# Optimization experiments

Measured on AMD Instinct MI355X. Metric: run time of the kernel, lower is better.

Reference implementation:

```python
import jax, jax.numpy as jnp
import numpy as np

D_MODEL = 1024
NUM_HEADS = 16
D_KEY = D_MODEL // NUM_HEADS


def setup_inputs() -> dict:
    key = jax.random.key(0)
    ks = jax.random.split(key, 9)
    B, S = 2, 2048
    s = 1.0 / np.sqrt(D_MODEL)
    return {
        "x": jax.random.normal(ks[0], (B, S, D_MODEL), dtype=jnp.float32),
        "W_q": jax.random.normal(ks[1], (D_MODEL, D_MODEL), dtype=jnp.float32) * s,
        "b_q": jnp.zeros((D_MODEL,), dtype=jnp.float32),
        "W_k": jax.random.normal(ks[2], (D_MODEL, D_MODEL), dtype=jnp.float32) * s,
        "b_k": jnp.zeros((D_MODEL,), dtype=jnp.float32),
        "W_v": jax.random.normal(ks[3], (D_MODEL, D_MODEL), dtype=jnp.float32) * s,
        "b_v": jnp.zeros((D_MODEL,), dtype=jnp.float32),
        "W_o": jax.random.normal(ks[4], (D_MODEL, D_MODEL), dtype=jnp.float32) * s,
        "b_o": jnp.zeros((D_MODEL,), dtype=jnp.float32),
    }


def reference(x, W_q, b_q, W_k, b_k, W_v, b_v, W_o, b_o):
    B, S, _ = x.shape
    # Linear projections (torch nn.Linear: x @ W.T + b; here W stored as [in, out])
    Q = x @ W_q + b_q
    K = x @ W_k + b_k
    V = x @ W_v + b_v
    # [B, S, H, dk] -> [B, H, S, dk]
    def split_heads(t):
        return t.reshape(B, S, NUM_HEADS, D_KEY).transpose(0, 2, 1, 3)
    Q, K, V = split_heads(Q), split_heads(K), split_heads(V)
    scale = 1.0 / np.sqrt(D_KEY).astype(np.float32)
    logits = jnp.einsum("bhqd,bhkd->bhqk", Q, K) * scale  # [B,H,S,S]
    weights = jax.nn.softmax(logits, axis=-1)
    ctx = jnp.einsum("bhqk,bhkd->bhqd", weights, V)       # [B,H,S,dk]
    concat = ctx.transpose(0, 2, 1, 3).reshape(B, S, D_MODEL)
    return concat @ W_o + b_o
```

## Files before the change

kernel.cpp:

```cpp
#include <hip/hip_runtime.h>
#include <cstdint>
#include <cstddef>

#define SEQ   2048
#define NH    16
#define DK    64
#define DM    1024
#define MTOT  4096
#define QSCALE (0.125f * 1.44269504088896f)

typedef __attribute__((ext_vector_type(8))) short           short8;
typedef __attribute__((ext_vector_type(8))) unsigned short  ushort8;
typedef __attribute__((ext_vector_type(4))) unsigned short  ushort4v;
typedef __attribute__((ext_vector_type(2))) unsigned int    uint2v;
typedef __attribute__((ext_vector_type(4))) unsigned int    uint4v;
typedef __attribute__((ext_vector_type(4))) float           float4v;
typedef unsigned short u16;
typedef unsigned int   u32;

__device__ inline float4v mfma16(short8 a, short8 b, float4v c) {
    return __builtin_amdgcn_mfma_f32_16x16x32_bf16(a, b, c, 0, 0, 0);
}
__device__ inline u16 f2bf(float f) {
    u32 u = __float_as_uint(f);
    u += 0x7fffu + ((u >> 16) & 1u);
    return (u16)(u >> 16);
}
__device__ inline u32 pkbf(float a, float b) {
    u32 r;
    asm("v_cvt_pk_bf16_f32 %0, %1, %2" : "=v"(r) : "v"(a), "v"(b));
    return r;
}
__device__ inline float ex2(float x) {
    float r;
    asm("v_exp_f32 %0, %1" : "=v"(r) : "v"(x));
    return r;
}
__device__ inline void pl32swap(u32& a, u32& b) {
    asm("v_permlane32_swap_b32 %0, %1" : "+v"(a), "+v"(b));
}
__device__ inline void pl16swap(u32& a, u32& b) {
    asm("v_permlane16_swap_b32 %0, %1" : "+v"(a), "+v"(b));
}
__device__ inline void gld16(const void* g, void* lds) {
    __builtin_amdgcn_global_load_lds(
        (const __attribute__((address_space(1))) u32*)g,
        (__attribute__((address_space(3))) u32*)lds, 16, 0, 0);
}

__global__ __launch_bounds__(256)
void convert_x(const float* __restrict__ x, u16* __restrict__ xb)
{
    const int i = blockIdx.x * 256 + threadIdx.x;
    const float4v a = ((const float4v*)x)[2 * i];
    const float4v b = ((const float4v*)x)[2 * i + 1];
    ushort8 o;
    #pragma unroll
    for (int j = 0; j < 4; j++) { o[j] = f2bf(a[j]); o[4 + j] = f2bf(b[j]); }
    ((ushort8*)xb)[i] = o;
}

__global__ __launch_bounds__(256)
void transpose_w(const float* __restrict__ W0, const float* __restrict__ W1,
                 const float* __restrict__ W2, const float* __restrict__ W3,
                 u16* __restrict__ T0, u16* __restrict__ T1,
                 u16* __restrict__ T2, u16* __restrict__ T3)
{
    __shared__ u16 t[64][68];
    const float* W; u16* T;
    switch (blockIdx.z) {
        case 0: W = W0; T = T0; break;
        case 1: W = W1; T = T1; break;
        case 2: W = W2; T = T2; break;
        default: W = W3; T = T3; break;
    }
    const int n0 = blockIdx.x * 64, k0 = blockIdx.y * 64;
    const int r  = threadIdx.x >> 4;
    const int c4 = (threadIdx.x & 15) * 4;
    #pragma unroll
    for (int i = 0; i < 4; i++) {
        float4v v = *(const float4v*)&W[(size_t)(k0 + r + i * 16) * DM + n0 + c4];
        #pragma unroll
        for (int j = 0; j < 4; j++) t[r + i * 16][c4 + j] = f2bf(v[j]);
    }
    __syncthreads();
    #pragma unroll
    for (int i = 0; i < 4; i++) {
        const int rr = r + i * 16;
        ushort4v o;
        #pragma unroll
        for (int j = 0; j < 4; j++) o[j] = t[c4 + j][rr];
        *(ushort4v*)&T[(size_t)(n0 + rr) * DM + k0 + c4] = o;
    }
}

template<int TM, int MODE>
__global__ __launch_bounds__(512)
void gemm_bt(const u16* __restrict__ A, const u16* __restrict__ WT,
             const float* __restrict__ bq, const float* __restrict__ bk,
             const float* __restrict__ bv,
             void* __restrict__ out0, u16* __restrict__ outK, u16* __restrict__ outV)
{
    constexpr int NT = 512;
    constexpr int MF = TM / 32;
    __shared__ u16 Al[2][TM][64];
    __shared__ u16 Bl[2][128][64];
    const int tid  = threadIdx.x;
    const int lane = tid & 63, w = tid >> 6;
    const int quad = lane >> 4, l16 = lane & 15;

    const int nxb  = gridDim.x;
    const int wgid = blockIdx.y * nxb + blockIdx.x;
    const int per  = (nxb * gridDim.y) >> 3;
    const int nl   = (wgid & 7) * per + (wgid >> 3);
    const int n0 = (nl % nxb) * 128, m0 = (nl / nxb) * TM;

    const int wm = (w >> 2) * (TM / 2);
    const int wn = (w & 3) * 32;

    float4v acc[MF][2] = {};

    auto STAGE = [&](int k0, int buf) {
        #pragma unroll
        for (int j = 0; j < TM * 8 / NT; j++) {
            const int c = j * NT + tid;
            const int row = c >> 3, kc = c & 7;
            gld16(A + (size_t)(m0 + row) * DM + k0 + ((kc ^ (row & 7)) * 8),
                  &Al[buf][0][0] + (size_t)(j * NT + w * 64) * 8);
        }
        #pragma unroll
        for (int j = 0; j < 1024 / NT; j++) {
            const int c = j * NT + tid;
            const int row = c >> 3, kc = c & 7;
            gld16(WT + (size_t)(n0 + row) * DM + k0 + ((kc ^ (row & 7)) * 8),
                  &Bl[buf][0][0] + (size_t)(j * NT + w * 64) * 8);
        }
    };

    STAGE(0, 0);
    for (int ks = 0; ks < DM / 64; ++ks) {
        const int buf = ks & 1;
        __syncthreads();
        if (ks + 1 < DM / 64) STAGE((ks + 1) * 64, buf ^ 1);
        #pragma unroll
        for (int u = 0; u < 2; u++) {
            short8 af[MF], bf[2];
            #pragma unroll
            for (int mi = 0; mi < MF; mi++) {
                const int row = wm + mi * 16 + l16;
                af[mi] = *(const short8*)&Al[buf][row][((4 * u + quad) ^ (row & 7)) * 8];
            }
            #pragma unroll
            for (int ni = 0; ni < 2; ni++) {
                const int row = wn + ni * 16 + l16;
                bf[ni] = *(const short8*)&Bl[buf][row][((4 * u + quad) ^ (row & 7)) * 8];
            }
            __builtin_amdgcn_s_setprio(1);
            #pragma unroll
            for (int mi = 0; mi < MF; mi++)
                #pragma unroll
                for (int ni = 0; ni < 2; ni++)
                    acc[mi][ni] = mfma16(af[mi], bf[ni], acc[mi][ni]);
            __builtin_amdgcn_s_setprio(0);
        }
    }

    if constexpr (MODE == 0) {
        float* out = (float*)out0;
        #pragma unroll
        for (int ni = 0; ni < 2; ni++) {
            const int col = n0 + wn + ni * 16 + l16;
            const float bb = bq[col];
            #pragma unroll
            for (int mi = 0; mi < MF; mi++)
                #pragma unroll
                for (int r = 0; r < 4; r++) {
                    const int row = m0 + wm + mi * 16 + quad * 4 + r;
                    out[(size_t)row * DM + col] = acc[mi][ni][r] + bb;
                }
        }
    } else {
        const int seg = n0 >> 10;
        u16* outp = (seg == 0) ? (u16*)out0 : (seg == 1 ? outK : outV);
        const float* bias = (seg == 0) ? bq : (seg == 1 ? bk : bv);
        const float scl = (seg == 0) ? QSCALE : 1.0f;
        if (seg < 2) {
            #pragma unroll
            for (int ni = 0; ni < 2; ni++) {
                const int col = (n0 & 1023) + wn + ni * 16 + l16;
                const float bb = bias[col];
                const int h = col >> 6, d = col & 63;
                #pragma unroll
                for (int mi = 0; mi < MF; mi++)
                    #pragma unroll
                    for (int r = 0; r < 4; r++) {
                        const int row = m0 + wm + mi * 16 + quad * 4 + r;
                        const int b = row >> 11, s = row & (SEQ - 1);
                        outp[(((size_t)(b * NH + h) * SEQ + s) << 6) + d] =
                            f2bf((acc[mi][ni][r] + bb) * scl);
                    }
            }
        } else {
            #pragma unroll
            for (int ni = 0; ni < 2; ni++) {
                const int col = (n0 & 1023) + wn + ni * 16 + l16;
                const float bb = bias[col];
                const int h = col >> 6, d = col & 63;
                #pragma unroll
                for (int mi = 0; mi < MF; mi++) {
                    const int row0 = m0 + wm + mi * 16 + quad * 4;
                    const int b = row0 >> 11, s = row0 & (SEQ - 1);
                    uint2v pv;
                    pv[0] = pkbf(acc[mi][ni][0] + bb, acc[mi][ni][1] + bb);
                    pv[1] = pkbf(acc[mi][ni][2] + bb, acc[mi][ni][3] + bb);
                    *(uint2v*)&outp[(((size_t)((b * NH + h) * DK + d)) << 11) + s] = pv;
                }
            }
        }
    }
}

__global__ __launch_bounds__(512, 4)
void attn_kernel(const u16* __restrict__ Q, const u16* __restrict__ K,
                 const u16* __restrict__ VT, u16* __restrict__ Ctx)
{
    __shared__ __align__(16) u16 pool[32768];

    const int tid  = threadIdx.x;
    const int lane = tid & 63, w = tid >> 6;
    const int wq = w & 3, wgrp = w >> 2;
    const int quad = lane >> 4, l16 = lane & 15;

    const int wgid = blockIdx.y * 16 + blockIdx.x;
    const int nlin = (wgid & 7) * 64 + (wgid >> 3);
    const int qt = nlin & 15;
    const int bh = nlin >> 4;
    const size_t head = (size_t)bh * SEQ * DK;

    short8 qf[2][2];
    #pragma unroll
    for (int g = 0; g < 2; g++) {
        const size_t qrow = head + (size_t)(qt * 128 + wq * 32 + g * 16 + l16) * DK;
        qf[g][0] = *(const short8*)(Q + qrow + quad * 8);
        qf[g][1] = *(const short8*)(Q + qrow + 32 + quad * 8);
    }

    float4v acc[2][4] = {};
    float l_part[2] = {0.f, 0.f};

    const int sh = tid >> 8;
    const int rK = (tid >> 3) & 31, cK = tid & 7;
    const int dV = (tid >> 2) & 63, cV = tid & 3;
    const int sVk = (dV & 3) ^ ((dV >> 2) & 3);
    const u16* const Kg = K  + head + (size_t)(sh * 1024 + rK) * DK + (cK ^ (rK & 7)) * 8;
    const u16* const Vg = VT + head + (size_t)dV * SEQ + sh * 1024 + (cV ^ sVk) * 8;
    u16* const Kdst = pool + tid * 8;
    u16* const Vdst = pool + 16384 + tid * 8;

    auto QKSTEP = [&](int cur, float4v znew[2][2]) {
        short8 kf[2][2];
        #pragma unroll
        for (int t = 0; t < 2; t++) {
            const int row = t * 16 + l16;
            const u16* kb = pool + cur * 4096 + wgrp * 2048 + row * 64;
            kf[t][0] = *(const short8*)(kb + (quad ^ (row & 7)) * 8);
            kf[t][1] = *(const short8*)(kb + ((4 + quad) ^ (row & 7)) * 8);
        }
        __builtin_amdgcn_s_setprio(1);
        #pragma unroll
        for (int t = 0; t < 2; t++)
            #pragma unroll
            for (int g = 0; g < 2; g++) {
                float4v zz = {};
                zz = mfma16(kf[t][0], qf[g][0], zz);
                zz = mfma16(kf[t][1], qf[g][1], zz);
                znew[t][g] = zz;
            }
        __builtin_amdgcn_s_setprio(0);
    };

    auto SMPACK = [&](float4v zp[2][2], short8 pf[2]) {
        #pragma unroll
        for (int g = 0; g < 2; g++) {
            float p[2][4];
            #pragma unroll
            for (int t = 0; t < 2; t++) {
                p[t][0] = ex2(zp[t][g][0]); p[t][1] = ex2(zp[t][g][1]);
                p[t][2] = ex2(zp[t][g][2]); p[t][3] = ex2(zp[t][g][3]);
                l_part[g] += (p[t][0] + p[t][1]) + (p[t][2] + p[t][3]);
            }
            u32 A = pkbf(p[0][0], p[0][1]);
            u32 B = pkbf(p[0][2], p[0][3]);
            u32 C = pkbf(p[1][0], p[1][1]);
            u32 D = pkbf(p[1][2], p[1][3]);
            pl32swap(A, C); pl16swap(A, C);
            pl32swap(B, D); pl16swap(B, D);
            uint4v pw; pw[0] = A; pw[1] = B; pw[2] = C; pw[3] = D;
            pf[g] = __builtin_bit_cast(short8, pw);
        }
    };

    auto PVSTEP = [&](int pv, short8 pf[2]) {
        __builtin_amdgcn_s_setprio(1);
        #pragma unroll
        for (int t = 0; t < 4; t++) {
            const int d = t * 16 + l16;
            const u16* vb = pool + 16384 + pv * 4096 + wgrp * 2048 + d * 32;
            const short8 vf =
                *(const short8*)(vb + (quad ^ ((d & 3) ^ ((d >> 2) & 3))) * 8);
            acc[0][t] = mfma16(vf, pf[0], acc[0][t]);
            acc[1][t] = mfma16(vf, pf[1], acc[1][t]);
        }
        __builtin_amdgcn_s_setprio(0);
    };

    gld16(Kg,                 Kdst);
    gld16(Vg,                 Vdst);
    gld16(Kg + 32 * DK,       Kdst + 4096);
    gld16(Vg + 32,            Vdst + 4096);

    float4v zp[2][2];

    __syncthreads();
    gld16(Kg + (size_t)2 * 32 * DK, Kdst + 2 * 4096);
    gld16(Vg + (size_t)2 * 32,      Vdst + 2 * 4096);
    QKSTEP(0, zp);

    for (int it = 1; it < 32; ++it) {
        const int cur = it & 3, pv = (it - 1) & 3;
        __syncthreads();
        if (it + 2 < 32) {
            gld16(Kg + (size_t)(it + 2) * 32 * DK, Kdst + ((it + 2) & 3) * 4096);
            gld16(Vg + (size_t)(it + 2) * 32,      Vdst + ((it + 2) & 3) * 4096);
        }
        float4v zn[2][2];
        QKSTEP(cur, zn);
        short8 pf[2];
        SMPACK(zp, pf);
        PVSTEP(pv, pf);
        #pragma unroll
        for (int t = 0; t < 2; t++)
            #pragma unroll
            for (int g = 0; g < 2; g++) zp[t][g] = zn[t][g];
    }
    {
        short8 pf[2];
        SMPACK(zp, pf);
        PVSTEP(3, pf);
    }

    #pragma unroll
    for (int g = 0; g < 2; g++) {
        l_part[g] += __shfl_xor(l_part[g], 16);
        l_part[g] += __shfl_xor(l_part[g], 32);
    }

    float* const Xlp = (float*)pool;
    #define XL(a, b, c) Xlp[(((a) * 64 + (b)) * 17) + (c)]
    float ltot[2];
    #pragma unroll
    for (int p = 0; p < 2; p++) {
        __syncthreads();
        if (wgrp == 1) {
            #pragma unroll
            for (int g = 0; g < 2; g++)
                #pragma unroll
                for (int tt = 0; tt < 2; tt++)
                    #pragma unroll
                    for (int r = 0; r < 4; r++)
                        XL(wq, lane, g * 8 + tt * 4 + r) = acc[g][2 * p + tt][r];
            XL(wq, lane, 16) = l_part[p];
        }
        __syncthreads();
        if (wgrp == 0) {
            #pragma unroll
            for (int g = 0; g < 2; g++)
                #pragma unroll
                for (int tt = 0; tt < 2; tt++)
                    #pragma unroll
                    for (int r = 0; r < 4; r++)
                        acc[g][2 * p + tt][r] += XL(wq, lane, g * 8 + tt * 4 + r);
            ltot[p] = l_part[p] + XL(wq, lane, 16);
        }
    }
    #undef XL

    if (wgrp == 0) {
        const int b = bh >> 4, h = bh & 15;
        #pragma unroll
        for (int g = 0; g < 2; g++) {
            const float rl = 1.0f / ltot[g];
            const int s = qt * 128 + wq * 32 + g * 16 + l16;
            u16* dst = Ctx + (size_t)(b * SEQ + s) * DM + h * 64 + quad * 4;
            #pragma unroll
            for (int t = 0; t < 4; t++) {
                uint2v ov;
                ov[0] = pkbf(acc[g][t][0] * rl, acc[g][t][1] * rl);
                ov[1] = pkbf(acc[g][t][2] * rl, acc[g][t][3] * rl);
                *(uint2v*)&dst[t * 16] = ov;
            }
        }
    }
}

extern "C" void kernel_launch(void* const* d_in, const int* in_sizes, int n_in,
                              void* d_out, int out_size, void* d_ws, size_t ws_size,
                              hipStream_t stream)
{
    const float* x   = (const float*)d_in[0];
    const float* W_q = (const float*)d_in[1];
    const float* b_q = (const float*)d_in[2];
    const float* W_k = (const float*)d_in[3];
    const float* b_k = (const float*)d_in[4];
    const float* W_v = (const float*)d_in[5];
    const float* b_v = (const float*)d_in[6];
    const float* W_o = (const float*)d_in[7];
    const float* b_o = (const float*)d_in[8];

    u16* xb  = (u16*)d_ws;
    u16* WT  = xb + (size_t)MTOT * DM;
    u16* WTo = WT + (size_t)3 * DM * DM;
    u16* VTb = WTo + (size_t)DM * DM;
    u16* Cb  = xb;
    u16* Qb  = (u16*)d_out;
    u16* Kb  = Qb + (size_t)MTOT * DM;

    convert_x<<<2048, 256, 0, stream>>>(x, xb);
    transpose_w<<<dim3(16, 16, 4), 256, 0, stream>>>(
        W_q, W_k, W_v, W_o, WT, WT + (size_t)DM * DM, WT + (size_t)2 * DM * DM, WTo);
    gemm_bt<128, 1><<<dim3(24, 32), 512, 0, stream>>>(xb, WT, b_q, b_k, b_v, Qb, Kb, VTb);
    attn_kernel<<<dim3(SEQ / 128, 2 * NH), 512, 0, stream>>>(Qb, Kb, VTb, Cb);
    gemm_bt<64, 0><<<dim3(8, 64), 512, 0, stream>>>(Cb, WTo, b_o, nullptr, nullptr,
                                                    (float*)d_out, nullptr, nullptr);
}
```

Before: 182.1 us.

## Fuse input prep kernels and widen QKV GEMM N-tile to 192

Merges the x-to-bf16 conversion and the weight transpose into one launch, removing one kernel launch and its tail. The QKV projection GEMM now uses a 192-wide N tile, giving a 16x32 grid of 512 blocks instead of 768 and more MFMA work per LDS load. The epilogue now picks the Q/K/V segment per fragment column, because a 192-wide tile can cross a 1024-column segment boundary. Wider tiles raise register and LDS use per block, which may lower occupancy.

```diff
diff --git a/kernel.cpp b/kernel.cpp
--- a/kernel.cpp
+++ b/kernel.cpp
@@ -49,32 +49,33 @@
 }
 
 __global__ __launch_bounds__(256)
-void convert_x(const float* __restrict__ x, u16* __restrict__ xb)
-{
-    const int i = blockIdx.x * 256 + threadIdx.x;
-    const float4v a = ((const float4v*)x)[2 * i];
-    const float4v b = ((const float4v*)x)[2 * i + 1];
-    ushort8 o;
-    #pragma unroll
-    for (int j = 0; j < 4; j++) { o[j] = f2bf(a[j]); o[4 + j] = f2bf(b[j]); }
-    ((ushort8*)xb)[i] = o;
-}
-
-__global__ __launch_bounds__(256)
-void transpose_w(const float* __restrict__ W0, const float* __restrict__ W1,
-                 const float* __restrict__ W2, const float* __restrict__ W3,
-                 u16* __restrict__ T0, u16* __restrict__ T1,
-                 u16* __restrict__ T2, u16* __restrict__ T3)
+void prep(const float* __restrict__ x, u16* __restrict__ xb,
+          const float* __restrict__ W0, const float* __restrict__ W1,
+          const float* __restrict__ W2, const float* __restrict__ W3,
+          u16* __restrict__ T0, u16* __restrict__ T1,
+          u16* __restrict__ T2, u16* __restrict__ T3)
 {
     __shared__ u16 t[64][68];
+    if (blockIdx.x < 2048) {
+        const int i = blockIdx.x * 256 + threadIdx.x;
+        const float4v a = ((const float4v*)x)[2 * i];
+        const float4v b = ((const float4v*)x)[2 * i + 1];
+        ushort8 o;
+        #pragma unroll
+        for (int j = 0; j < 4; j++) { o[j] = f2bf(a[j]); o[4 + j] = f2bf(b[j]); }
+        ((ushort8*)xb)[i] = o;
+        return;
+    }
+    const int bi = blockIdx.x - 2048;
+    const int bx = bi & 15, by = (bi >> 4) & 15, bz = bi >> 8;
     const float* W; u16* T;
-    switch (blockIdx.z) {
+    switch (bz) {
         case 0: W = W0; T = T0; break;
         case 1: W = W1; T = T1; break;
         case 2: W = W2; T = T2; break;
         default: W = W3; T = T3; break;
     }
-    const int n0 = blockIdx.x * 64, k0 = blockIdx.y * 64;
+    const int n0 = bx * 64, k0 = by * 64;
     const int r  = threadIdx.x >> 4;
     const int c4 = (threadIdx.x & 15) * 4;
     #pragma unroll
@@ -94,7 +95,7 @@
     }
 }
 
-template<int TM, int MODE>
+template<int TM, int BN, int MODE>
 __global__ __launch_bounds__(512)
 void gemm_bt(const u16* __restrict__ A, const u16* __restrict__ WT,
              const float* __restrict__ bq, const float* __restrict__ bk,
@@ -103,8 +104,9 @@
 {
     constexpr int NT = 512;
     constexpr int MF = TM / 32;
+    constexpr int NF = BN / 64;
     __shared__ u16 Al[2][TM][64];
-    __shared__ u16 Bl[2][128][64];
+    __shared__ u16 Bl[2][BN][64];
     const int tid  = threadIdx.x;
     const int lane = tid & 63, w = tid >> 6;
     const int quad = lane >> 4, l16 = lane & 15;
@@ -113,12 +115,12 @@
     const int wgid = blockIdx.y * nxb + blockIdx.x;
     const int per  = (nxb * gridDim.y) >> 3;
     const int nl   = (wgid & 7) * per + (wgid >> 3);
-    const int n0 = (nl % nxb) * 128, m0 = (nl / nxb) * TM;
+    const int n0 = (nl % nxb) * BN, m0 = (nl / nxb) * TM;
 
     const int wm = (w >> 2) * (TM / 2);
-    const int wn = (w & 3) * 32;
-
-    float4v acc[MF][2] = {};
+    const int wn = (w & 3) * (BN / 4);
+
+    float4v acc[MF][NF] = {};
 
     auto STAGE = [&](int k0, int buf) {
         #pragma unroll
@@ -129,7 +131,7 @@
                   &Al[buf][0][0] + (size_t)(j * NT + w * 64) * 8);
         }
         #pragma unroll
-        for (int j = 0; j < 1024 / NT; j++) {
+        for (int j = 0; j < BN * 8 / NT; j++) {
             const int c = j * NT + tid;
             const int row = c >> 3, kc = c & 7;
             gld16(WT + (size_t)(n0 + row) * DM + k0 + ((kc ^ (row & 7)) * 8),
@@ -144,14 +146,14 @@
         if (ks + 1 < DM / 64) STAGE((ks + 1) * 64, buf ^ 1);
         #pragma unroll
         for (int u = 0; u < 2; u++) {
-            short8 af[MF], bf[2];
+            short8 af[MF], bf[NF];
             #pragma unroll
             for (int mi = 0; mi < MF; mi++) {
                 const int row = wm + mi * 16 + l16;
                 af[mi] = *(const short8*)&Al[buf][row][((4 * u + quad) ^ (row & 7)) * 8];
             }
             #pragma unroll
-            for (int ni = 0; ni < 2; ni++) {
+            for (int ni = 0; ni < NF; ni++) {
                 const int row = wn + ni * 16 + l16;
                 bf[ni] = *(const short8*)&Bl[buf][row][((4 * u + quad) ^ (row & 7)) * 8];
             }
@@ -159,7 +161,7 @@
             #pragma unroll
             for (int mi = 0; mi < MF; mi++)
                 #pragma unroll
-                for (int ni = 0; ni < 2; ni++)
+                for (int ni = 0; ni < NF; ni++)
                     acc[mi][ni] = mfma16(af[mi], bf[ni], acc[mi][ni]);
             __builtin_amdgcn_s_setprio(0);
         }
@@ -168,7 +170,7 @@
     if constexpr (MODE == 0) {
         float* out = (float*)out0;
         #pragma unroll
-        for (int ni = 0; ni < 2; ni++) {
+        for (int ni = 0; ni < NF; ni++) {
             const int col = n0 + wn + ni * 16 + l16;
             const float bb = bq[col];
             #pragma unroll
@@ -180,16 +182,17 @@
                 }
         }
     } else {
-        const int seg = n0 >> 10;
-        u16* outp = (seg == 0) ? (u16*)out0 : (seg == 1 ? outK : outV);
-        const float* bias = (seg == 0) ? bq : (seg == 1 ? bk : bv);
-        const float scl = (seg == 0) ? QSCALE : 1.0f;
-        if (seg < 2) {
-            #pragma unroll
-            for (int ni = 0; ni < 2; ni++) {
-                const int col = (n0 & 1023) + wn + ni * 16 + l16;
-                const float bb = bias[col];
-                const int h = col >> 6, d = col & 63;
+        #pragma unroll
+        for (int ni = 0; ni < NF; ni++) {
+            const int colg = n0 + wn + ni * 16 + l16;
+            const int seg  = colg >> 10;
+            u16* outp = (seg == 0) ? (u16*)out0 : (seg == 1 ? outK : outV);
+            const float* bias = (seg == 0) ? bq : (seg == 1 ? bk : bv);
+            const int col = colg & 1023;
+            const float bb = bias[col];
+            const int h = col >> 6, d = col & 63;
+            if (seg < 2) {
+                const float scl = (seg == 0) ? QSCALE : 1.0f;
                 #pragma unroll
                 for (int mi = 0; mi < MF; mi++)
                     #pragma unroll
@@ -199,13 +202,7 @@
                         outp[(((size_t)(b * NH + h) * SEQ + s) << 6) + d] =
                             f2bf((acc[mi][ni][r] + bb) * scl);
                     }
-            }
-        } else {
-            #pragma unroll
-            for (int ni = 0; ni < 2; ni++) {
-                const int col = (n0 & 1023) + wn + ni * 16 + l16;
-                const float bb = bias[col];
-                const int h = col >> 6, d = col & 63;
+            } else {
                 #pragma unroll
                 for (int mi = 0; mi < MF; mi++) {
                     const int row0 = m0 + wm + mi * 16 + quad * 4;
@@ -425,11 +422,12 @@
     u16* Qb  = (u16*)d_out;
     u16* Kb  = Qb + (size_t)MTOT * DM;
 
-    convert_x<<<2048, 256, 0, stream>>>(x, xb);
-    transpose_w<<<dim3(16, 16, 4), 256, 0, stream>>>(
-        W_q, W_k, W_v, W_o, WT, WT + (size_t)DM * DM, WT + (size_t)2 * DM * DM, WTo);
-    gemm_bt<128, 1><<<dim3(24, 32), 512, 0, stream>>>(xb, WT, b_q, b_k, b_v, Qb, Kb, VTb);
+    prep<<<3072, 256, 0, stream>>>(x, xb, W_q, W_k, W_v, W_o,
+                                   WT, WT + (size_t)DM * DM,
+                                   WT + (size_t)2 * DM * DM, WTo);
+    gemm_bt<128, 192, 1><<<dim3(16, 32), 512, 0, stream>>>(
+        xb, WT, b_q, b_k, b_v, Qb, Kb, VTb);
     attn_kernel<<<dim3(SEQ / 128, 2 * NH), 512, 0, stream>>>(Qb, Kb, VTb, Cb);
-    gemm_bt<64, 0><<<dim3(8, 64), 512, 0, stream>>>(Cb, WTo, b_o, nullptr, nullptr,
-                                                    (float*)d_out, nullptr, nullptr);
-}
+    gemm_bt<64, 128, 0><<<dim3(8, 64), 512, 0, stream>>>(
+        Cb, WTo, b_o, nullptr, nullptr, (float*)d_out, nullptr, nullptr);
+}
```

New measurement: 175.2 us. 1.04x faster.
